# Kernel tuning notes

Measured on AMD Instinct MI355X. Metric: run time of the kernel, lower is better.

The kernel has to match this reference:

```python
import jax, jax.numpy as jnp
import numpy as np

E = 1024          # n_embed_dim
H = 64            # head_size = n_embed_dim // n_heads (16)

def setup_inputs() -> dict:
    key = jax.random.key(0)
    k_x, k_q, k_k, k_v = jax.random.split(key, 4)
    scale = 1.0 / np.sqrt(E)
    return {
        "x": jax.random.normal(k_x, (4, 2048, E), dtype=jnp.float32),
        "ln_gamma": jnp.ones((E,), jnp.float32),
        "ln_beta": jnp.zeros((E,), jnp.float32),
        # torch nn.Linear weights: [out_features, in_features]
        "Wq": jax.random.normal(k_q, (H, E), dtype=jnp.float32) * scale,
        "Wk": jax.random.normal(k_k, (H, E), dtype=jnp.float32) * scale,
        "Wv": jax.random.normal(k_v, (H, E), dtype=jnp.float32) * scale,
    }

def reference(x, ln_gamma, ln_beta, Wq, Wk, Wv):
    # LayerNorm over last dim (eps matches torch default 1e-5)
    mu = jnp.mean(x, axis=-1, keepdims=True)
    var = jnp.mean(jnp.square(x - mu), axis=-1, keepdims=True)
    xn = (x - mu) * jax.lax.rsqrt(var + 1e-5) * ln_gamma + ln_beta

    q = jnp.einsum('bse,he->bsh', xn, Wq)   # [B,S,H]
    k = jnp.einsum('bse,he->bsh', xn, Wk)
    v = jnp.einsum('bse,he->bsh', xn, Wv)

    scores = jnp.einsum('bqh,bkh->bqk', q, k) / jnp.sqrt(jnp.float32(H))
    S = x.shape[1]
    causal = jnp.tril(jnp.ones((S, S), dtype=bool))
    scores = jnp.where(causal, scores, -jnp.inf)
    attn = jax.nn.softmax(scores, axis=-1)
    return jnp.einsum('bqk,bkh->bqh', attn, v)
```

## Files before the change

### kernel.cpp

```cpp
#include <hip/hip_runtime.h>

#define E 1024
#define HH 64
#define BB 4
#define SS 2048
#define BS (BB*SS)
#define NSLOT 144

typedef unsigned short u16;
typedef short bf16x8 __attribute__((ext_vector_type(8)));
typedef float f32x4 __attribute__((ext_vector_type(4)));

#define LOG2E_O8 0.18033688011112042f

__device__ inline u16 f2bf(float f) {
    unsigned int u = __float_as_uint(f);
    unsigned int r = (u + 0x7FFFu + ((u >> 16) & 1u)) >> 16;
    return (u16)r;
}
__device__ inline float bf2f(u16 h) {
    return __uint_as_float(((unsigned int)h) << 16);
}

__global__ __launch_bounds__(256) void ln_wcast(const float* __restrict__ x,
        const float* __restrict__ gamma, const float* __restrict__ beta,
        const float* __restrict__ Wq, const float* __restrict__ Wk,
        const float* __restrict__ Wv,
        u16* __restrict__ xn, u16* __restrict__ wc) {
    const int t = threadIdx.x;
    if (blockIdx.x < 2048) {
        const int w = t >> 6, lane = t & 63;
        const size_t row = (size_t)blockIdx.x * 4 + w;
        const float4* xr = (const float4*)(x + row * E);
        float4 v[4];
        #pragma unroll
        for (int i = 0; i < 4; ++i) v[i] = xr[lane + 64 * i];
        float s = 0.f, sq = 0.f;
        #pragma unroll
        for (int i = 0; i < 4; ++i) {
            s  += v[i].x + v[i].y + v[i].z + v[i].w;
            sq += v[i].x*v[i].x + v[i].y*v[i].y + v[i].z*v[i].z + v[i].w*v[i].w;
        }
        #pragma unroll
        for (int off = 32; off > 0; off >>= 1) {
            s  += __shfl_xor(s,  off);
            sq += __shfl_xor(sq, off);
        }
        const float mean = s * (1.0f / E);
        const float var  = sq * (1.0f / E) - mean * mean;
        const float rstd = rsqrtf(var + 1e-5f);
        const float4* gr = (const float4*)gamma;
        const float4* br = (const float4*)beta;
        #pragma unroll
        for (int i = 0; i < 4; ++i) {
            const float4 g  = gr[lane + 64 * i];
            const float4 bt = br[lane + 64 * i];
            ushort4 o;
            o.x = f2bf((v[i].x - mean) * rstd * g.x + bt.x);
            o.y = f2bf((v[i].y - mean) * rstd * g.y + bt.y);
            o.z = f2bf((v[i].z - mean) * rstd * g.z + bt.z);
            o.w = f2bf((v[i].w - mean) * rstd * g.w + bt.w);
            *(ushort4*)(xn + row * E + (lane + 64 * i) * 4) = o;
        }
    } else {
        const int row = blockIdx.x - 2048;
        const float* src = (row < 64)  ? (Wq + (size_t)row * E)
                         : (row < 128) ? (Wk + (size_t)(row - 64) * E)
                                       : (Wv + (size_t)(row - 128) * E);
        const float sc = (row < 64) ? LOG2E_O8 : 1.0f;
        const float4 v = *(const float4*)(src + t * 4);
        ushort4 o;
        o.x = f2bf(v.x * sc); o.y = f2bf(v.y * sc);
        o.z = f2bf(v.z * sc); o.w = f2bf(v.w * sc);
        *(ushort4*)(wc + (size_t)row * E + t * 4) = o;
    }
}

__global__ __launch_bounds__(256) void qkv_mfma(const u16* __restrict__ xn,
        const u16* __restrict__ wc,
        u16* __restrict__ qb, u16* __restrict__ kb, u16* __restrict__ vt) {
    const int mb   = blockIdx.x >> 1;
    const int half = blockIdx.x & 1;
    const int row0 = mb * 32;
    const int t = threadIdx.x;
    const int w = t >> 6, lane = t & 63;
    const int quad = lane >> 4, r15 = lane & 15;
    const int mt = w >> 1, cgrp = w & 1;
    __shared__ u16 Xs[32 * 64];
    __shared__ u16 Ws[96 * 64];
    f32x4 acc[3] = {};

    for (int kc = 0; kc < E; kc += 64) {
        __syncthreads();
        {
            const int row = t >> 3, ch = t & 7;
            const uint4 d = *(const uint4*)(xn + (size_t)(row0 + row) * E + kc + ch * 8);
            *(uint4*)&Xs[row * 64 + (ch ^ (row & 7)) * 8] = d;
        }
        #pragma unroll
        for (int i = 0; i < 3; ++i) {
            const int idx = i * 256 + t;
            const int wl = idx >> 3, ch = idx & 7;
            const uint4 d = *(const uint4*)(wc + (size_t)(half * 96 + wl) * E + kc + ch * 8);
            *(uint4*)&Ws[wl * 64 + (ch ^ (wl & 7)) * 8] = d;
        }
        __syncthreads();
        #pragma unroll
        for (int kk = 0; kk < 2; ++kk) {
            const int xrow = mt * 16 + r15;
            const bf16x8 af = *(const bf16x8*)&Xs[xrow * 64 + ((kk * 4 + quad) ^ (xrow & 7)) * 8];
            #pragma unroll
            for (int j = 0; j < 3; ++j) {
                const int wl = (cgrp * 3 + j) * 16 + r15;
                const bf16x8 bfr = *(const bf16x8*)&Ws[wl * 64 + ((kk * 4 + quad) ^ (wl & 7)) * 8];
                acc[j] = __builtin_amdgcn_mfma_f32_16x16x32_bf16(af, bfr, acc[j], 0, 0, 0);
            }
        }
    }
    const int b    = row0 >> 11;
    const int key0 = row0 & 2047;
    #pragma unroll
    for (int j = 0; j < 3; ++j) {
        const int cg  = half * 96 + cgrp * 48 + j * 16 + r15;
        const int sel = cg >> 6;
        const int col = cg & 63;
        if (sel < 2) {
            u16* base = (sel == 0) ? qb : kb;
            #pragma unroll
            for (int r = 0; r < 4; ++r) {
                const size_t row = (size_t)row0 + mt * 16 + quad * 4 + r;
                base[row * HH + col] = f2bf(acc[j][r]);
            }
        } else {
            ushort4 pk;
            pk.x = f2bf(acc[j][0]); pk.y = f2bf(acc[j][1]);
            pk.z = f2bf(acc[j][2]); pk.w = f2bf(acc[j][3]);
            *(ushort4*)(vt + (size_t)b * HH * SS + (size_t)col * SS
                           + key0 + mt * 16 + quad * 4) = pk;
        }
    }
}

__global__ __launch_bounds__(256) void attn_partial(const u16* __restrict__ qb,
        const u16* __restrict__ kb, const u16* __restrict__ vt,
        u16* __restrict__ po, float* __restrict__ pl,
        float* __restrict__ out) {
    const int bid = blockIdx.x;
    const int b   = bid >> 8;
    const int rem = bid & 255;
    const int qt  = rem >> 3, c = rem & 7;
    const int a   = qt >> 2;
    if (c > a) return;
    const int nc   = a + 1;
    const int r_   = qt & 3;
    const int slot = b * NSLOT + 2 * a * (a + 1) + r_ * (a + 1) + c;
    const int q0   = qt << 6;
    const int t = threadIdx.x;
    const int w = t >> 6, lane = t & 63;
    const int quad = lane >> 4, r15 = lane & 15;

    __shared__ u16 Ks[64 * 64];
    __shared__ u16 VT[64 * 64];
    __shared__ u16 Ps[64 * 64];

    const size_t qrow = ((size_t)b * SS + q0 + w * 16 + r15) * HH;
    const bf16x8 qf0 = *(const bf16x8*)(qb + qrow + quad * 8);
    const bf16x8 qf1 = *(const bf16x8*)(qb + qrow + 32 + quad * 8);

    f32x4 o[4] = {};
    float l_[4] = {0.f, 0.f, 0.f, 0.f};

    const int t1 = min(c * 4 + 4, qt + 1);
    for (int tile = c * 4; tile < t1; ++tile) {
        const int kt = tile << 6;
        __syncthreads();
        {
            const int row = t >> 2, ch0 = (t & 3) * 2;
            const uint4* src = (const uint4*)(kb + ((size_t)b * SS + kt + row) * HH + ch0 * 8);
            const uint4 d0 = src[0], d1 = src[1];
            *(uint4*)&Ks[row * 64 + ((ch0    ) ^ (row & 7)) * 8] = d0;
            *(uint4*)&Ks[row * 64 + ((ch0 + 1) ^ (row & 7)) * 8] = d1;
        }
        {
            const int h = t >> 2, ch0 = (t & 3) * 2;
            const uint4* src = (const uint4*)(vt + (size_t)b * HH * SS + (size_t)h * SS + kt + ch0 * 8);
            const uint4 d0 = src[0], d1 = src[1];
            *(uint4*)&VT[h * 64 + ((ch0    ) ^ (h & 7)) * 8] = d0;
            *(uint4*)&VT[h * 64 + ((ch0 + 1) ^ (h & 7)) * 8] = d1;
        }
        __syncthreads();

        f32x4 s[4] = {};
        #pragma unroll
        for (int nt = 0; nt < 4; ++nt) {
            const int krow = nt * 16 + r15;
            const bf16x8 k0 = *(const bf16x8*)&Ks[krow * 64 + ((    quad) ^ (krow & 7)) * 8];
            const bf16x8 k1 = *(const bf16x8*)&Ks[krow * 64 + ((4 + quad) ^ (krow & 7)) * 8];
            s[nt] = __builtin_amdgcn_mfma_f32_16x16x32_bf16(qf0, k0, s[nt], 0, 0, 0);
            s[nt] = __builtin_amdgcn_mfma_f32_16x16x32_bf16(qf1, k1, s[nt], 0, 0, 0);
        }
        if (tile == qt) {
            #pragma unroll
            for (int nt = 0; nt < 4; ++nt)
                #pragma unroll
                for (int r = 0; r < 4; ++r)
                    if (nt * 16 + r15 > w * 16 + quad * 4 + r) s[nt][r] = -INFINITY;
        }

        float p[4][4];
        #pragma unroll
        for (int r = 0; r < 4; ++r) {
            #pragma unroll
            for (int nt = 0; nt < 4; ++nt)
                p[nt][r] = __builtin_amdgcn_exp2f(s[nt][r]);
            l_[r] += (p[0][r] + p[1][r]) + (p[2][r] + p[3][r]);
        }

        #pragma unroll
        for (int nt = 0; nt < 4; ++nt)
            #pragma unroll
            for (int r = 0; r < 4; ++r) {
                const int prow = w * 16 + quad * 4 + r;
                const int col  = nt * 16 + r15;
                Ps[prow * 64 + (((col >> 3) ^ (prow & 7)) * 8) + (col & 7)] = f2bf(p[nt][r]);
            }
        const int arow = w * 16 + r15;
        const bf16x8 pf0 = *(const bf16x8*)&Ps[arow * 64 + ((    quad) ^ (arow & 7)) * 8];
        const bf16x8 pf1 = *(const bf16x8*)&Ps[arow * 64 + ((4 + quad) ^ (arow & 7)) * 8];

        #pragma unroll
        for (int ht = 0; ht < 4; ++ht) {
            const int vrow = ht * 16 + r15;
            const bf16x8 v0 = *(const bf16x8*)&VT[vrow * 64 + ((    quad) ^ (vrow & 7)) * 8];
            const bf16x8 v1 = *(const bf16x8*)&VT[vrow * 64 + ((4 + quad) ^ (vrow & 7)) * 8];
            o[ht] = __builtin_amdgcn_mfma_f32_16x16x32_bf16(pf0, v0, o[ht], 0, 0, 0);
            o[ht] = __builtin_amdgcn_mfma_f32_16x16x32_bf16(pf1, v1, o[ht], 0, 0, 0);
        }
    }

    #pragma unroll
    for (int r = 0; r < 4; ++r) {
        l_[r] += __shfl_xor(l_[r], 1); l_[r] += __shfl_xor(l_[r], 2);
        l_[r] += __shfl_xor(l_[r], 4); l_[r] += __shfl_xor(l_[r], 8);
    }

    if (nc == 1) {
        #pragma unroll
        for (int r = 0; r < 4; ++r) {
            const float inv = 1.0f / l_[r];
            const size_t orow = ((size_t)b * SS + q0 + w * 16 + quad * 4 + r) * HH;
            #pragma unroll
            for (int ht = 0; ht < 4; ++ht)
                out[orow + ht * 16 + r15] = o[ht][r] * inv;
        }
        return;
    }
    #pragma unroll
    for (int r = 0; r < 4; ++r) {
        const int q = w * 16 + quad * 4 + r;
        #pragma unroll
        for (int ht = 0; ht < 4; ++ht)
            po[(size_t)slot * 4096 + q * 64 + ht * 16 + r15] = f2bf(o[ht][r]);
        if (r15 == 0) pl[slot * 64 + q] = l_[r];
    }
}

__global__ __launch_bounds__(256) void attn_reduce(const u16* __restrict__ po,
        const float* __restrict__ pl, float* __restrict__ out) {
    const int bid = blockIdx.x;
    const int b = bid >> 7, rem = bid & 127;
    const int qt = rem >> 2, qq = rem & 3;
    if (qt < 4) return;
    const int a = qt >> 2, r_ = qt & 3;
    const int nc = a + 1;
    const int sbase = b * NSLOT + 2 * a * (a + 1) + r_ * (a + 1);
    const int t = threadIdx.x;
    const int h = t & 63, qr = t >> 6;
    #pragma unroll
    for (int i = 0; i < 4; ++i) {
        const int q = qq * 16 + qr * 4 + i;
        float osum = 0.f, lsum = 0.f;
        for (int cidx = 0; cidx < nc; ++cidx) {
            osum += bf2f(po[(size_t)(sbase + cidx) * 4096 + q * 64 + h]);
            lsum += pl[(sbase + cidx) * 64 + q];
        }
        out[((size_t)b * SS + (qt << 6) + q) * HH + h] = osum / lsum;
    }
}

extern "C" void kernel_launch(void* const* d_in, const int* in_sizes, int n_in,
                              void* d_out, int out_size, void* d_ws, size_t ws_size,
                              hipStream_t stream) {
    const float* x     = (const float*)d_in[0];
    const float* gamma = (const float*)d_in[1];
    const float* beta  = (const float*)d_in[2];
    const float* Wq    = (const float*)d_in[3];
    const float* Wk    = (const float*)d_in[4];
    const float* Wv    = (const float*)d_in[5];
    float* out = (float*)d_out;

    char* p = (char*)d_ws;
    u16*   xn   = (u16*)p;                         p += (size_t)BS * E * 2;
    u16*   wc   = (u16*)p;                         p += 393216;
    u16*   qb   = (u16*)p;                         p += (size_t)BS * HH * 2;
    u16*   kb   = (u16*)p;                         p += (size_t)BS * HH * 2;
    u16*   vt   = (u16*)p;                         p += (size_t)BS * HH * 2;
    u16*   po   = (u16*)p;                         p += (size_t)BB * NSLOT * 4096 * 2;
    float* pl   = (float*)p;

    ln_wcast    <<<2048 + 192,  256, 0, stream>>>(x, gamma, beta, Wq, Wk, Wv, xn, wc);
    qkv_mfma    <<<BS / 16,     256, 0, stream>>>(xn, wc, qb, kb, vt);
    attn_partial<<<BB * 32 * 8, 256, 0, stream>>>(qb, kb, vt, po, pl, out);
    attn_reduce <<<BB * 32 * 4, 256, 0, stream>>>(po, pl, out);
}
```

Before: 122.7 us.

## Preload all K/V tiles into LDS up front and widen QKV K-chunks

The attention partial kernel now loads every K and V tile for its chunk (up to four) into a larger LDS buffer in one phase with a single barrier. It then runs the score/softmax/PV loop with no per-tile global loads or barriers. The QKV projection kernel now stages 128-wide K chunks instead of 64, which halves the number of loop iterations and barrier pairs. Both changes cut synchronisation and let more global loads be in flight at once. The cost is much more LDS per block (about 72 KB in attention), which can lower occupancy.

```diff
diff --git a/kernel.cpp b/kernel.cpp
--- a/kernel.cpp
+++ b/kernel.cpp
@@ -86,33 +86,40 @@
     const int w = t >> 6, lane = t & 63;
     const int quad = lane >> 4, r15 = lane & 15;
     const int mt = w >> 1, cgrp = w & 1;
-    __shared__ u16 Xs[32 * 64];
-    __shared__ u16 Ws[96 * 64];
+    __shared__ u16 Xs[32 * 128];
+    __shared__ u16 Ws[96 * 128];
     f32x4 acc[3] = {};
-
-    for (int kc = 0; kc < E; kc += 64) {
+    const int xrow = mt * 16 + r15;
+
+    for (int kc8 = 0; kc8 < 8; ++kc8) {
         __syncthreads();
         {
             const int row = t >> 3, ch = t & 7;
-            const uint4 d = *(const uint4*)(xn + (size_t)(row0 + row) * E + kc + ch * 8);
-            *(uint4*)&Xs[row * 64 + (ch ^ (row & 7)) * 8] = d;
-        }
-        #pragma unroll
-        for (int i = 0; i < 3; ++i) {
+            #pragma unroll
+            for (int hf = 0; hf < 2; ++hf) {
+                const uint4 d = *(const uint4*)(xn + (size_t)(row0 + row) * E
+                                                + kc8 * 128 + hf * 64 + ch * 8);
+                *(uint4*)&Xs[row * 128 + hf * 64 + (ch ^ (row & 7)) * 8] = d;
+            }
+        }
+        #pragma unroll
+        for (int i = 0; i < 6; ++i) {
             const int idx = i * 256 + t;
-            const int wl = idx >> 3, ch = idx & 7;
-            const uint4 d = *(const uint4*)(wc + (size_t)(half * 96 + wl) * E + kc + ch * 8);
-            *(uint4*)&Ws[wl * 64 + (ch ^ (wl & 7)) * 8] = d;
+            const int wl = idx >> 4, ch16 = idx & 15;
+            const int hf = ch16 >> 3, ch = ch16 & 7;
+            const uint4 d = *(const uint4*)(wc + (size_t)(half * 96 + wl) * E
+                                            + kc8 * 128 + hf * 64 + ch * 8);
+            *(uint4*)&Ws[wl * 128 + hf * 64 + (ch ^ (wl & 7)) * 8] = d;
         }
         __syncthreads();
         #pragma unroll
-        for (int kk = 0; kk < 2; ++kk) {
-            const int xrow = mt * 16 + r15;
-            const bf16x8 af = *(const bf16x8*)&Xs[xrow * 64 + ((kk * 4 + quad) ^ (xrow & 7)) * 8];
+        for (int kk = 0; kk < 4; ++kk) {
+            const int hf = kk >> 1, q4 = (kk & 1) * 4 + quad;
+            const bf16x8 af = *(const bf16x8*)&Xs[xrow * 128 + hf * 64 + (q4 ^ (xrow & 7)) * 8];
             #pragma unroll
             for (int j = 0; j < 3; ++j) {
                 const int wl = (cgrp * 3 + j) * 16 + r15;
-                const bf16x8 bfr = *(const bf16x8*)&Ws[wl * 64 + ((kk * 4 + quad) ^ (wl & 7)) * 8];
+                const bf16x8 bfr = *(const bf16x8*)&Ws[wl * 128 + hf * 64 + (q4 ^ (wl & 7)) * 8];
                 acc[j] = __builtin_amdgcn_mfma_f32_16x16x32_bf16(af, bfr, acc[j], 0, 0, 0);
             }
         }
@@ -159,43 +166,47 @@
     const int w = t >> 6, lane = t & 63;
     const int quad = lane >> 4, r15 = lane & 15;
 
-    __shared__ u16 Ks[64 * 64];
-    __shared__ u16 VT[64 * 64];
+    __shared__ u16 Ks[4 * 64 * 64];
+    __shared__ u16 VT[4 * 64 * 64];
     __shared__ u16 Ps[64 * 64];
 
     const size_t qrow = ((size_t)b * SS + q0 + w * 16 + r15) * HH;
     const bf16x8 qf0 = *(const bf16x8*)(qb + qrow + quad * 8);
     const bf16x8 qf1 = *(const bf16x8*)(qb + qrow + 32 + quad * 8);
 
+    const int ntiles = min(c * 4 + 4, qt + 1) - c * 4;
+
+    {
+        const int row = t >> 2, ch0 = (t & 3) * 2;
+        for (int tl = 0; tl < ntiles; ++tl) {
+            const int kt = (c * 4 + tl) << 6;
+            const uint4* srcK = (const uint4*)(kb + ((size_t)b * SS + kt + row) * HH + ch0 * 8);
+            const uint4 k0 = srcK[0], k1 = srcK[1];
+            *(uint4*)&Ks[tl * 4096 + row * 64 + ((ch0    ) ^ (row & 7)) * 8] = k0;
+            *(uint4*)&Ks[tl * 4096 + row * 64 + ((ch0 + 1) ^ (row & 7)) * 8] = k1;
+            const uint4* srcV = (const uint4*)(vt + (size_t)b * HH * SS + (size_t)row * SS
+                                               + kt + ch0 * 8);
+            const uint4 v0 = srcV[0], v1 = srcV[1];
+            *(uint4*)&VT[tl * 4096 + row * 64 + ((ch0    ) ^ (row & 7)) * 8] = v0;
+            *(uint4*)&VT[tl * 4096 + row * 64 + ((ch0 + 1) ^ (row & 7)) * 8] = v1;
+        }
+    }
+    __syncthreads();
+
     f32x4 o[4] = {};
     float l_[4] = {0.f, 0.f, 0.f, 0.f};
 
-    const int t1 = min(c * 4 + 4, qt + 1);
-    for (int tile = c * 4; tile < t1; ++tile) {
-        const int kt = tile << 6;
-        __syncthreads();
-        {
-            const int row = t >> 2, ch0 = (t & 3) * 2;
-            const uint4* src = (const uint4*)(kb + ((size_t)b * SS + kt + row) * HH + ch0 * 8);
-            const uint4 d0 = src[0], d1 = src[1];
-            *(uint4*)&Ks[row * 64 + ((ch0    ) ^ (row & 7)) * 8] = d0;
-            *(uint4*)&Ks[row * 64 + ((ch0 + 1) ^ (row & 7)) * 8] = d1;
-        }
-        {
-            const int h = t >> 2, ch0 = (t & 3) * 2;
-            const uint4* src = (const uint4*)(vt + (size_t)b * HH * SS + (size_t)h * SS + kt + ch0 * 8);
-            const uint4 d0 = src[0], d1 = src[1];
-            *(uint4*)&VT[h * 64 + ((ch0    ) ^ (h & 7)) * 8] = d0;
-            *(uint4*)&VT[h * 64 + ((ch0 + 1) ^ (h & 7)) * 8] = d1;
-        }
-        __syncthreads();
+    for (int tl = 0; tl < ntiles; ++tl) {
+        const int tile = c * 4 + tl;
+        const u16* KsT = &Ks[tl * 4096];
+        const u16* VTT = &VT[tl * 4096];
 
         f32x4 s[4] = {};
         #pragma unroll
         for (int nt = 0; nt < 4; ++nt) {
             const int krow = nt * 16 + r15;
-            const bf16x8 k0 = *(const bf16x8*)&Ks[krow * 64 + ((    quad) ^ (krow & 7)) * 8];
-            const bf16x8 k1 = *(const bf16x8*)&Ks[krow * 64 + ((4 + quad) ^ (krow & 7)) * 8];
+            const bf16x8 k0 = *(const bf16x8*)&KsT[krow * 64 + ((    quad) ^ (krow & 7)) * 8];
+            const bf16x8 k1 = *(const bf16x8*)&KsT[krow * 64 + ((4 + quad) ^ (krow & 7)) * 8];
             s[nt] = __builtin_amdgcn_mfma_f32_16x16x32_bf16(qf0, k0, s[nt], 0, 0, 0);
             s[nt] = __builtin_amdgcn_mfma_f32_16x16x32_bf16(qf1, k1, s[nt], 0, 0, 0);
         }
@@ -231,8 +242,8 @@
         #pragma unroll
         for (int ht = 0; ht < 4; ++ht) {
             const int vrow = ht * 16 + r15;
-            const bf16x8 v0 = *(const bf16x8*)&VT[vrow * 64 + ((    quad) ^ (vrow & 7)) * 8];
-            const bf16x8 v1 = *(const bf16x8*)&VT[vrow * 64 + ((4 + quad) ^ (vrow & 7)) * 8];
+            const bf16x8 v0 = *(const bf16x8*)&VTT[vrow * 64 + ((    quad) ^ (vrow & 7)) * 8];
+            const bf16x8 v1 = *(const bf16x8*)&VTT[vrow * 64 + ((4 + quad) ^ (vrow & 7)) * 8];
             o[ht] = __builtin_amdgcn_mfma_f32_16x16x32_bf16(pf0, v0, o[ht], 0, 0, 0);
             o[ht] = __builtin_amdgcn_mfma_f32_16x16x32_bf16(pf1, v1, o[ht], 0, 0, 0);
         }
```

After: 121.3 us. About the same (-1.2%).
